# Optimization experiments

Measured on AMD Instinct MI355X. Metric: run time of the kernel, lower is better.

Reference implementation:

```python
import jax, jax.numpy as jnp
import numpy as np

B, S, D, H = 4, 2048, 1024, 16
HD = D // H  # head dim = 64
NEG = jnp.finfo(jnp.float32).min


def setup_inputs() -> dict:
    key = jax.random.key(0)
    ks = jax.random.split(key, 6)
    states = jax.random.normal(ks[0], (B, S, D), dtype=jnp.float32)
    # causal float mask, broadcastable over batch and heads
    mask = jnp.tril(jnp.ones((S, S), dtype=jnp.float32))[None, None, :, :]
    scale = 1.0 / np.sqrt(D)
    Wq = jax.random.normal(ks[1], (D, D), dtype=jnp.float32) * scale
    Wk = jax.random.normal(ks[2], (D, D), dtype=jnp.float32) * scale
    Wv = jax.random.normal(ks[3], (D, D), dtype=jnp.float32) * scale
    Wo = jax.random.normal(ks[4], (D, D), dtype=jnp.float32) * scale
    return {"states": states, "mask": mask, "Wq": Wq, "Wk": Wk, "Wv": Wv, "Wo": Wo}


def _split_heads(x):
    # [B,S,D] -> [B,H,S,HD]
    return x.reshape(B, S, H, HD).transpose(0, 2, 1, 3)


def reference(states, mask, Wq, Wk, Wv, Wo):
    q = _split_heads(states @ Wq)
    k = _split_heads(states @ Wk)
    v = _split_heads(states @ Wv)
    # scores [B,H,S,S], scaled by rsqrt(head_dim) as in the original
    alpha = jnp.einsum("bhqd,bhkd->bhqk", q, k) * (1.0 / jnp.sqrt(jnp.float32(HD)))
    alpha = alpha * mask + (1.0 - mask) * NEG
    alpha = jax.nn.softmax(alpha, axis=-1)
    ctx = jnp.einsum("bhqk,bhkd->bhqd", alpha, v)
    ctx = ctx.transpose(0, 2, 1, 3).reshape(B, S, D)  # concat heads
    return ctx @ Wo
```

## Files before the change

kernel.cpp:

```cpp
#include <hip/hip_runtime.h>
#include <hip/hip_bf16.h>

#define BB 4
#define SS 2048
#define DD 1024
#define HH 16
#define HDD 64
#define MM (BB*SS)

typedef __attribute__((ext_vector_type(8))) short short8;
typedef __attribute__((ext_vector_type(4))) float f32x4;
typedef __attribute__((ext_vector_type(4))) int int4v;
typedef __attribute__((ext_vector_type(4))) short bf16x4;

__device__ __forceinline__ ushort f2bf(float f) {
  union { float f; uint u; } v; v.f = f;
  uint u = v.u;
  uint r = (u + 0x7FFFu + ((u >> 16) & 1u)) >> 16;
  return (ushort)r;
}

__device__ __forceinline__ float exp2f_fast(float x) {
#if __has_builtin(__builtin_amdgcn_exp2f)
  return __builtin_amdgcn_exp2f(x);
#else
  float r; asm("v_exp_f32 %0, %1" : "=v"(r) : "v"(x)); return r;
#endif
}

__device__ __forceinline__ bf16x4 pack4bf(float a, float b, float c, float d) {
  union { __hip_bfloat162 h2[2]; bf16x4 s; } u;
  u.h2[0] = __float22bfloat162_rn(make_float2(a, b));
  u.h2[1] = __float22bfloat162_rn(make_float2(c, d));
  return u.s;
}

__device__ __forceinline__ f32x4 mfma16(bf16x4 a, bf16x4 b, f32x4 c) {
#if __has_builtin(__builtin_amdgcn_mfma_f32_16x16x16bf16_1k)
  return __builtin_amdgcn_mfma_f32_16x16x16bf16_1k(a, b, c, 0, 0, 0);
#else
  f32x4 d;
  asm volatile("s_nop 1\n\tv_mfma_f32_16x16x16_bf16 %0, %1, %2, %3\n\ts_nop 7\n\ts_nop 3"
               : "=v"(d) : "v"(a), "v"(b), "v"(c));
  return d;
#endif
}

__device__ __forceinline__ void gload16(void* lds, const void* g) {
  __builtin_amdgcn_global_load_lds((const __attribute__((address_space(1))) void*)g,
                                   (__attribute__((address_space(3))) void*)lds, 16, 0, 0);
}

__global__ __launch_bounds__(256) void k_prep(const float* __restrict__ states, ushort* __restrict__ Xbf,
                                              const float* __restrict__ W0, const float* __restrict__ W1,
                                              const float* __restrict__ W2, const float* __restrict__ W3,
                                              ushort* __restrict__ T0, ushort* __restrict__ T1,
                                              ushort* __restrict__ T2, ushort* __restrict__ T3) {
  int bid = blockIdx.x;
  int tid = threadIdx.x;
  if (bid >= 4096) {
    int i = (bid - 4096) * 256 + tid;
    float4 v = ((const float4*)states)[i];
    uint lo = (uint)f2bf(v.x) | ((uint)f2bf(v.y) << 16);
    uint hi = (uint)f2bf(v.z) | ((uint)f2bf(v.w) << 16);
    ((uint2*)Xbf)[i] = make_uint2(lo, hi);
    return;
  }
  __shared__ float t[32][33];
  int bz = bid >> 10;
  int by = (bid >> 5) & 31, bx = bid & 31;
  const float* W; ushort* T;
  switch (bz) {
    case 0: W = W0; T = T0; break;
    case 1: W = W1; T = T1; break;
    case 2: W = W2; T = T2; break;
    default: W = W3; T = T3; break;
  }
  float scale = (bz == 0) ? 0.18033688011112042f : 1.0f;
  int tx = tid & 31, ty = tid >> 5;
  int x = bx * 32 + tx;
  int y0 = by * 32;
#pragma unroll
  for (int j = 0; j < 32; j += 8) t[ty + j][tx] = W[(y0 + ty + j) * DD + x];
  __syncthreads();
#pragma unroll
  for (int j = 0; j < 32; j += 8)
    T[(bx * 32 + ty + j) * DD + y0 + tx] = f2bf(t[tx][ty + j] * scale);
}

__global__ __launch_bounds__(256, 2) void k_qkv(const ushort* __restrict__ X,
                                                const ushort* __restrict__ Wqt,
                                                const ushort* __restrict__ Wkt,
                                                const ushort* __restrict__ Wvt,
                                                ushort* __restrict__ Q,
                                                ushort* __restrict__ K,
                                                ushort* __restrict__ Vt) {
  __shared__ ushort Al[2 * 4096];
  __shared__ ushort Bl[3][2 * 4096];
  int tid = threadIdx.x, lane = tid & 63, w = tid >> 6;
  int wm = w >> 1, wn = w & 1, lrow = lane & 15, lgrp = lane >> 4;
  int srow = lane >> 2, scolb = (lane & 3) * 16;
  const char* A8 = (const char*)(X + (size_t)blockIdx.x * 128 * DD);
  const char* B8[3] = { (const char*)(Wqt + (size_t)blockIdx.y * 128 * DD),
                        (const char*)(Wkt + (size_t)blockIdx.y * 128 * DD),
                        (const char*)(Wvt + (size_t)blockIdx.y * 128 * DD) };

  f32x4 acc[3][4][4];
#pragma unroll
  for (int wi = 0; wi < 3; wi++)
#pragma unroll
    for (int i = 0; i < 4; i++)
#pragma unroll
      for (int j = 0; j < 4; j++)
#pragma unroll
        for (int r = 0; r < 4; r++) acc[wi][i][j][r] = 0.f;

#pragma unroll
  for (int ii = 0; ii < 2; ii++) {
    int i = w * 2 + ii;
    size_t ro = (size_t)(i * 16 + srow) * (DD * 2) + scolb;
    gload16(Al + i * 512, A8 + ro);
#pragma unroll
    for (int wi = 0; wi < 3; wi++)
      gload16(&Bl[wi][i * 512], B8[wi] + ro);
  }
  __syncthreads();

  for (int kk = 0; kk < DD; kk += 32) {
    int cur = (kk >> 5) & 1;
    if (kk + 32 < DD) {
#pragma unroll
      for (int ii = 0; ii < 2; ii++) {
        int i = w * 2 + ii;
        size_t ro = (size_t)(i * 16 + srow) * (DD * 2) + (kk + 32) * 2 + scolb;
        gload16(Al + (cur ^ 1) * 4096 + i * 512, A8 + ro);
#pragma unroll
        for (int wi = 0; wi < 3; wi++)
          gload16(&Bl[wi][(cur ^ 1) * 4096 + i * 512], B8[wi] + ro);
      }
    }
    short8 a[4];
#pragma unroll
    for (int i = 0; i < 4; i++)
      a[i] = *(const short8*)&Al[cur * 4096 + (wm * 64 + i * 16 + lrow) * 32 + lgrp * 8];
#pragma unroll
    for (int wi = 0; wi < 3; wi++) {
      short8 b[4];
#pragma unroll
      for (int j = 0; j < 4; j++)
        b[j] = *(const short8*)&Bl[wi][cur * 4096 + (wn * 64 + j * 16 + lrow) * 32 + lgrp * 8];
#pragma unroll
      for (int i = 0; i < 4; i++)
#pragma unroll
        for (int j = 0; j < 4; j++)
          acc[wi][i][j] = __builtin_amdgcn_mfma_f32_16x16x32_bf16(a[i], b[j], acc[wi][i][j], 0, 0, 0);
    }
    __syncthreads();
  }

  int m0 = blockIdx.x * 128 + wm * 64, n0 = blockIdx.y * 128 + wn * 64;
#pragma unroll
  for (int wi = 0; wi < 2; wi++) {
    ushort* Out = (wi == 0) ? Q : K;
#pragma unroll
    for (int i = 0; i < 4; i++)
#pragma unroll
      for (int j = 0; j < 4; j++)
#pragma unroll
        for (int r = 0; r < 4; r++) {
          int row = m0 + i * 16 + lgrp * 4 + r;
          int col = n0 + j * 16 + lrow;
          int b = row >> 11, s = row & 2047, h = col >> 6, hd = col & 63;
          Out[(((size_t)(b * HH + h) * SS) + s) * HDD + hd] = f2bf(acc[wi][i][j][r]);
        }
  }
#pragma unroll
  for (int i = 0; i < 4; i++)
#pragma unroll
    for (int j = 0; j < 4; j++) {
      int row0 = m0 + i * 16 + lgrp * 4;
      int col = n0 + j * 16 + lrow;
      int b = row0 >> 11, s0 = row0 & 2047, h = col >> 6, hd = col & 63;
      bf16x4 s = pack4bf(acc[2][i][j][0], acc[2][i][j][1], acc[2][i][j][2], acc[2][i][j][3]);
      *(bf16x4*)(Vt + (((size_t)(b * HH + h) * HDD) + hd) * SS + s0) = s;
    }
}

#define QB2 64
#define KVB 64
#define NQT2 (SS / QB2)

__global__ __launch_bounds__(128) void k_attn(const ushort* __restrict__ Q,
                                              const ushort* __restrict__ K,
                                              const ushort* __restrict__ Vt,
                                              ushort* __restrict__ Ctx) {
  __shared__ ushort Kl[2][4096];
  __shared__ ushort Vl[2][4096];
  int bid = blockIdx.x;
  int xcd = bid & 7, slot = bid >> 3;
  int j = slot & 15;
  int bh = (slot >> 4) * 8 + xcd;
  int b = bh >> 4, h = bh & 15;
  int tid = threadIdx.x, lane = tid & 63, w = tid >> 6;
  int lrow = lane & 15, lgrp = lane >> 4;

  int srow = lane >> 3;
  int scolb = ((lane & 7) * 16) ^ (srow << 4);
  const char* K8 = (const char*)(K + (size_t)bh * SS * HDD);
  const char* V8 = (const char*)(Vt + (size_t)bh * HDD * SS);

  int kswz = (lrow & 7) << 3;
  int colE[2];
  colE[0] = (lgrp * 8) ^ kswz;
  colE[1] = (lgrp * 8 + 32) ^ kswz;

  const ushort* kc0 = &Kl[0][lrow * 64 + colE[0]];
  const ushort* kc1 = &Kl[0][lrow * 64 + colE[1]];
  const ushort* vbp[4];
#pragma unroll
  for (int t = 0; t < 4; t++) vbp[t] = &Vl[0][lrow * 64 + (((16 * t + lgrp * 4) ^ kswz))];

#pragma unroll
  for (int ph = 0; ph < 2; ph++) {
    int qx = ph == 0 ? (NQT2 - 1 - j) : j;
    int qb = qx * QB2;
    int qw0 = qb + w * 32;
    int ntk = qx + 1;

    const char* kgp[4];
    const char* vgp[4];
#pragma unroll
    for (int ii = 0; ii < 4; ii++) {
      kgp[ii] = K8 + (size_t)(w * 32 + ii * 8 + srow) * 128 + scolb;
      vgp[ii] = V8 + (size_t)(w * 32 + ii * 8 + srow) * (SS * 2) + scolb;
    }

    short8 qf[2][2];
#pragma unroll
    for (int qt = 0; qt < 2; qt++)
#pragma unroll
      for (int c = 0; c < 2; c++)
        qf[qt][c] = *(const short8*)(Q + ((size_t)bh * SS + qb + w * 32 + qt * 16 + lrow) * HDD + lgrp * 8 + 32 * c);

    f32x4 o[2][4];
#pragma unroll
    for (int qt = 0; qt < 2; qt++)
#pragma unroll
      for (int nt = 0; nt < 4; nt++)
#pragma unroll
        for (int r = 0; r < 4; r++) o[qt][nt][r] = 0.f;
    float l_run[2] = {0.f, 0.f};

#pragma unroll
    for (int ii = 0; ii < 4; ii++) {
      gload16(&Kl[0][(w * 4 + ii) * 512], kgp[ii]);
      gload16(&Vl[0][(w * 4 + ii) * 512], vgp[ii]);
      kgp[ii] += KVB * 128;
      vgp[ii] += KVB * 2;
    }
    __syncthreads();

    for (int kt = 0; kt < ntk; kt++) {
      int cur = kt & 1;
      if (kt + 1 < ntk) {
#pragma unroll
        for (int ii = 0; ii < 4; ii++) {
          gload16(&Kl[cur ^ 1][(w * 4 + ii) * 512], kgp[ii]);
          gload16(&Vl[cur ^ 1][(w * 4 + ii) * 512], vgp[ii]);
          kgp[ii] += KVB * 128;
          vgp[ii] += KVB * 2;
        }
      }
      int kb = kt * KVB;
      const ushort* kcc0 = kc0 + (cur << 12);
      const ushort* kcc1 = kc1 + (cur << 12);
      short8 kf[4][2];
#pragma unroll
      for (int t = 0; t < 4; t++) {
        kf[t][0] = *(const short8*)(kcc0 + t * 1024);
        kf[t][1] = *(const short8*)(kcc1 + t * 1024);
      }

      bf16x4 pk[2][4];
#pragma unroll
      for (int qt = 0; qt < 2; qt++) {
        f32x4 st[4];
#pragma unroll
        for (int t = 0; t < 4; t++) {
          f32x4 z;
#pragma unroll
          for (int r = 0; r < 4; r++) z[r] = 0.f;
          z = __builtin_amdgcn_mfma_f32_16x16x32_bf16(kf[t][0], qf[qt][0], z, 0, 0, 0);
          z = __builtin_amdgcn_mfma_f32_16x16x32_bf16(kf[t][1], qf[qt][1], z, 0, 0, 0);
          st[t] = z;
        }
        if (kb + 63 > qw0) {
          int lim = qw0 + qt * 16 + lrow - kb - lgrp * 4;
#pragma unroll
          for (int t = 0; t < 4; t++)
#pragma unroll
            for (int r = 0; r < 4; r++)
              if (16 * t + r > lim) st[t][r] = -1e30f;
        }
        float rs = 0.f;
#pragma unroll
        for (int t = 0; t < 4; t++) {
          float e0 = exp2f_fast(st[t][0] - 8.f);
          float e1 = exp2f_fast(st[t][1] - 8.f);
          float e2 = exp2f_fast(st[t][2] - 8.f);
          float e3 = exp2f_fast(st[t][3] - 8.f);
          rs += (e0 + e1) + (e2 + e3);
          pk[qt][t] = pack4bf(e0, e1, e2, e3);
        }
        l_run[qt] += rs;
      }

#pragma unroll
      for (int t = 0; t < 4; t++) {
        const ushort* vbt = vbp[t] + (cur << 12);
#pragma unroll
        for (int nt = 0; nt < 4; nt++) {
          bf16x4 va = *(const bf16x4*)(vbt + nt * 1024);
          o[0][nt] = mfma16(va, pk[0][t], o[0][nt]);
          o[1][nt] = mfma16(va, pk[1][t], o[1][nt]);
        }
      }
      __syncthreads();
    }

#pragma unroll
    for (int qt = 0; qt < 2; qt++) {
      float lt = l_run[qt];
      lt += __shfl_xor(lt, 16);
      lt += __shfl_xor(lt, 32);
      float inv = 1.f / lt;
      int q = qb + w * 32 + qt * 16 + lrow;
      ushort* base = Ctx + ((size_t)b * SS + q) * DD + h * HDD;
#pragma unroll
      for (int nt = 0; nt < 4; nt++) {
        bf16x4 s = pack4bf(o[qt][nt][0] * inv, o[qt][nt][1] * inv,
                           o[qt][nt][2] * inv, o[qt][nt][3] * inv);
        *(bf16x4*)(base + nt * 16 + lgrp * 4) = s;
      }
    }
  }
}

__global__ __launch_bounds__(256) void k_oproj(const ushort* __restrict__ Ctx,
                                               const ushort* __restrict__ Wot,
                                               float* __restrict__ Outp) {
  __shared__ ushort Al[2][8192];
  __shared__ ushort Bl[2][8192];
  int tid = threadIdx.x, lane = tid & 63, w = tid >> 6;
  int wm = w >> 1, wn = w & 1, lrow = lane & 15, lgrp = lane >> 4;
  int srow = lane >> 3;
  int scolb = ((lane & 7) * 16) ^ (srow << 4);
  const char* A8 = (const char*)(Ctx + (size_t)blockIdx.x * 128 * DD);
  const char* B8 = (const char*)(Wot + (size_t)blockIdx.y * 128 * DD);

  f32x4 acc[4][4];
#pragma unroll
  for (int i = 0; i < 4; i++)
#pragma unroll
    for (int j = 0; j < 4; j++)
#pragma unroll
      for (int r = 0; r < 4; r++) acc[i][j][r] = 0.f;

  int aswz = (lrow & 7) << 3;
  int colA[2], colB[2];
#pragma unroll
  for (int k2 = 0; k2 < 2; k2++) {
    colA[k2] = (k2 * 32 + lgrp * 8) ^ aswz;
    colB[k2] = (k2 * 32 + lgrp * 8) ^ aswz;
  }

#pragma unroll
  for (int ii = 0; ii < 4; ii++) {
    int i = w * 4 + ii;
    size_t ro = (size_t)(i * 8 + srow) * (DD * 2) + scolb;
    gload16(&Al[0][i * 512], A8 + ro);
    gload16(&Bl[0][i * 512], B8 + ro);
  }
  __syncthreads();

  for (int kk = 0; kk < DD; kk += 64) {
    int cur = (kk >> 6) & 1;
    if (kk + 64 < DD) {
#pragma unroll
      for (int ii = 0; ii < 4; ii++) {
        int i = w * 4 + ii;
        size_t ro = (size_t)(i * 8 + srow) * (DD * 2) + (kk + 64) * 2 + scolb;
        gload16(&Al[cur ^ 1][i * 512], A8 + ro);
        gload16(&Bl[cur ^ 1][i * 512], B8 + ro);
      }
    }
    short8 a[4][2], bfr[4][2];
#pragma unroll
    for (int i = 0; i < 4; i++)
#pragma unroll
      for (int k2 = 0; k2 < 2; k2++)
        a[i][k2] = *(const short8*)&Al[cur][(wm * 64 + i * 16 + lrow) * 64 + colA[k2]];
#pragma unroll
    for (int jj = 0; jj < 4; jj++)
#pragma unroll
      for (int k2 = 0; k2 < 2; k2++)
        bfr[jj][k2] = *(const short8*)&Bl[cur][(wn * 64 + jj * 16 + lrow) * 64 + colB[k2]];
#pragma unroll
    for (int i = 0; i < 4; i++)
#pragma unroll
      for (int jj = 0; jj < 4; jj++) {
        acc[i][jj] = __builtin_amdgcn_mfma_f32_16x16x32_bf16(a[i][0], bfr[jj][0], acc[i][jj], 0, 0, 0);
        acc[i][jj] = __builtin_amdgcn_mfma_f32_16x16x32_bf16(a[i][1], bfr[jj][1], acc[i][jj], 0, 0, 0);
      }
    __syncthreads();
  }

  int m0 = blockIdx.x * 128 + wm * 64, n0 = blockIdx.y * 128 + wn * 64;
#pragma unroll
  for (int i = 0; i < 4; i++)
#pragma unroll
    for (int j = 0; j < 4; j++)
#pragma unroll
      for (int r = 0; r < 4; r++) {
        int row = m0 + i * 16 + lgrp * 4 + r;
        int col = n0 + j * 16 + lrow;
        Outp[(size_t)row * DD + col] = acc[i][j][r];
      }
}

extern "C" void kernel_launch(void* const* d_in, const int* in_sizes, int n_in,
                              void* d_out, int out_size, void* d_ws, size_t ws_size,
                              hipStream_t stream) {
  const float* states = (const float*)d_in[0];
  const float* Wq = (const float*)d_in[2];
  const float* Wk = (const float*)d_in[3];
  const float* Wv = (const float*)d_in[4];
  const float* Wo = (const float*)d_in[5];
  float* outp = (float*)d_out;

  char* ws = (char*)d_ws;
  const size_t XBF = 0;
  const size_t WQT = 16777216;
  const size_t WKT = WQT + 2097152;
  const size_t WVT = WKT + 2097152;
  const size_t WOT = WVT + 2097152;
  const size_t QO  = WOT + 2097152;
  const size_t KO  = QO + 16777216;
  const size_t VT  = KO + 16777216;
  const size_t CTX = VT + 16777216;

  ushort* Xbf = (ushort*)(ws + XBF);
  ushort* Wqt = (ushort*)(ws + WQT);
  ushort* Wkt = (ushort*)(ws + WKT);
  ushort* Wvt = (ushort*)(ws + WVT);
  ushort* Wot = (ushort*)(ws + WOT);
  ushort* Qb  = (ushort*)(ws + QO);
  ushort* Kb  = (ushort*)(ws + KO);
  ushort* Vtb = (ushort*)(ws + VT);
  ushort* Ctb = (ushort*)(ws + CTX);

  k_prep<<<dim3(4096 + MM * DD / 4 / 256), 256, 0, stream>>>(
      states, Xbf, Wq, Wk, Wv, Wo, Wqt, Wkt, Wvt, Wot);
  k_qkv<<<dim3(MM / 128, DD / 128), 256, 0, stream>>>(Xbf, Wqt, Wkt, Wvt, Qb, Kb, Vtb);
  k_attn<<<dim3(NQT2 * BB * HH / 2), 128, 0, stream>>>(Qb, Kb, Vtb, Ctb);
  k_oproj<<<dim3(MM / 128, DD / 128), 256, 0, stream>>>(Ctb, Wot, outp);
}
```

Measured before the change: 158.1 us.

## Deepen attention K/V pipeline to four 32-key stages with explicit vmcnt waits

The attention kernel now processes 32-key tiles through a four-slot shared-memory ring, prefetching three tiles ahead. It replaces the trailing __syncthreads with explicit s_waitcnt vmcnt plus a single s_barrier per iteration. The V tile layout and swizzle are reworked for 32-column tiles. This aims to hide global-load latency better in the latency-bound attention loop, at the cost of twice as many loop iterations and barriers and hand-tuned wait counts that must match the load count. The oproj changes are cosmetic: colB is merged into colA and the grid expression is rewritten to the same value.

```diff
diff --git a/kernel.cpp b/kernel.cpp
--- a/kernel.cpp
+++ b/kernel.cpp
@@ -187,15 +187,15 @@
 }
 
 #define QB2 64
-#define KVB 64
+#define KVB3 32
 #define NQT2 (SS / QB2)
 
 __global__ __launch_bounds__(128) void k_attn(const ushort* __restrict__ Q,
                                               const ushort* __restrict__ K,
                                               const ushort* __restrict__ Vt,
                                               ushort* __restrict__ Ctx) {
-  __shared__ ushort Kl[2][4096];
-  __shared__ ushort Vl[2][4096];
+  __shared__ ushort Kl[4][2048];
+  __shared__ ushort Vl[4][2048];
   int bid = blockIdx.x;
   int xcd = bid & 7, slot = bid >> 3;
   int j = slot & 15;
@@ -206,6 +206,8 @@
 
   int srow = lane >> 3;
   int scolb = ((lane & 7) * 16) ^ (srow << 4);
+  int vrow = lane >> 2;
+  int vcolb = ((lane & 3) * 16) ^ ((vrow & 3) << 4);
   const char* K8 = (const char*)(K + (size_t)bh * SS * HDD);
   const char* V8 = (const char*)(Vt + (size_t)bh * HDD * SS);
 
@@ -216,23 +218,22 @@
 
   const ushort* kc0 = &Kl[0][lrow * 64 + colE[0]];
   const ushort* kc1 = &Kl[0][lrow * 64 + colE[1]];
-  const ushort* vbp[4];
-#pragma unroll
-  for (int t = 0; t < 4; t++) vbp[t] = &Vl[0][lrow * 64 + (((16 * t + lgrp * 4) ^ kswz))];
+  const ushort* vb0 = &Vl[0][lrow * 32 + (( 0 + 4 * lgrp) ^ ((lrow & 3) << 3))];
+  const ushort* vb1 = &Vl[0][lrow * 32 + ((16 + 4 * lgrp) ^ ((lrow & 3) << 3))];
 
 #pragma unroll
   for (int ph = 0; ph < 2; ph++) {
     int qx = ph == 0 ? (NQT2 - 1 - j) : j;
     int qb = qx * QB2;
     int qw0 = qb + w * 32;
-    int ntk = qx + 1;
-
-    const char* kgp[4];
-    const char* vgp[4];
-#pragma unroll
-    for (int ii = 0; ii < 4; ii++) {
-      kgp[ii] = K8 + (size_t)(w * 32 + ii * 8 + srow) * 128 + scolb;
-      vgp[ii] = V8 + (size_t)(w * 32 + ii * 8 + srow) * (SS * 2) + scolb;
+    int ntk = 2 * (qx + 1);
+
+    const char* kgp[2];
+    const char* vgp[2];
+#pragma unroll
+    for (int ii = 0; ii < 2; ii++) {
+      kgp[ii] = K8 + (size_t)((w * 2 + ii) * 8 + srow) * 128 + scolb;
+      vgp[ii] = V8 + (size_t)((w * 2 + ii) * 16 + vrow) * (SS * 2) + vcolb;
     }
 
     short8 qf[2][2];
@@ -240,7 +241,7 @@
     for (int qt = 0; qt < 2; qt++)
 #pragma unroll
       for (int c = 0; c < 2; c++)
-        qf[qt][c] = *(const short8*)(Q + ((size_t)bh * SS + qb + w * 32 + qt * 16 + lrow) * HDD + lgrp * 8 + 32 * c);
+        qf[qt][c] = *(const short8*)(Q + ((size_t)bh * SS + qw0 + qt * 16 + lrow) * HDD + lgrp * 8 + 32 * c);
 
     f32x4 o[2][4];
 #pragma unroll
@@ -251,42 +252,52 @@
         for (int r = 0; r < 4; r++) o[qt][nt][r] = 0.f;
     float l_run[2] = {0.f, 0.f};
 
-#pragma unroll
-    for (int ii = 0; ii < 4; ii++) {
-      gload16(&Kl[0][(w * 4 + ii) * 512], kgp[ii]);
-      gload16(&Vl[0][(w * 4 + ii) * 512], vgp[ii]);
-      kgp[ii] += KVB * 128;
-      vgp[ii] += KVB * 2;
-    }
-    __syncthreads();
+    int npro = ntk < 3 ? ntk : 3;
+    for (int s = 0; s < npro; s++) {
+#pragma unroll
+      for (int ii = 0; ii < 2; ii++) {
+        gload16(&Kl[s][(w * 2 + ii) * 512], kgp[ii]);
+        gload16(&Vl[s][(w * 2 + ii) * 512], vgp[ii]);
+        kgp[ii] += KVB3 * 128;
+        vgp[ii] += KVB3 * 2;
+      }
+    }
 
     for (int kt = 0; kt < ntk; kt++) {
-      int cur = kt & 1;
-      if (kt + 1 < ntk) {
-#pragma unroll
-        for (int ii = 0; ii < 4; ii++) {
-          gload16(&Kl[cur ^ 1][(w * 4 + ii) * 512], kgp[ii]);
-          gload16(&Vl[cur ^ 1][(w * 4 + ii) * 512], vgp[ii]);
-          kgp[ii] += KVB * 128;
-          vgp[ii] += KVB * 2;
+      int rem = ntk - kt;
+      if (rem >= 3)      { asm volatile("s_waitcnt vmcnt(8)" ::: "memory"); }
+      else if (rem == 2) { asm volatile("s_waitcnt vmcnt(4)" ::: "memory"); }
+      else               { asm volatile("s_waitcnt vmcnt(0)" ::: "memory"); }
+      __builtin_amdgcn_sched_barrier(0);
+      __builtin_amdgcn_s_barrier();
+      __builtin_amdgcn_sched_barrier(0);
+      if (kt + 3 < ntk) {
+        int nb = (kt + 3) & 3;
+#pragma unroll
+        for (int ii = 0; ii < 2; ii++) {
+          gload16(&Kl[nb][(w * 2 + ii) * 512], kgp[ii]);
+          gload16(&Vl[nb][(w * 2 + ii) * 512], vgp[ii]);
+          kgp[ii] += KVB3 * 128;
+          vgp[ii] += KVB3 * 2;
         }
       }
-      int kb = kt * KVB;
-      const ushort* kcc0 = kc0 + (cur << 12);
-      const ushort* kcc1 = kc1 + (cur << 12);
-      short8 kf[4][2];
-#pragma unroll
-      for (int t = 0; t < 4; t++) {
+      int buf = kt & 3;
+      int kb = kt * KVB3;
+      const ushort* kcc0 = kc0 + (buf << 11);
+      const ushort* kcc1 = kc1 + (buf << 11);
+      short8 kf[2][2];
+#pragma unroll
+      for (int t = 0; t < 2; t++) {
         kf[t][0] = *(const short8*)(kcc0 + t * 1024);
         kf[t][1] = *(const short8*)(kcc1 + t * 1024);
       }
 
-      bf16x4 pk[2][4];
+      bf16x4 pk[2][2];
 #pragma unroll
       for (int qt = 0; qt < 2; qt++) {
-        f32x4 st[4];
-#pragma unroll
-        for (int t = 0; t < 4; t++) {
+        f32x4 st[2];
+#pragma unroll
+        for (int t = 0; t < 2; t++) {
           f32x4 z;
 #pragma unroll
           for (int r = 0; r < 4; r++) z[r] = 0.f;
@@ -294,17 +305,17 @@
           z = __builtin_amdgcn_mfma_f32_16x16x32_bf16(kf[t][1], qf[qt][1], z, 0, 0, 0);
           st[t] = z;
         }
-        if (kb + 63 > qw0) {
+        if (kb + 31 > qw0) {
           int lim = qw0 + qt * 16 + lrow - kb - lgrp * 4;
 #pragma unroll
-          for (int t = 0; t < 4; t++)
+          for (int t = 0; t < 2; t++)
 #pragma unroll
             for (int r = 0; r < 4; r++)
               if (16 * t + r > lim) st[t][r] = -1e30f;
         }
         float rs = 0.f;
 #pragma unroll
-        for (int t = 0; t < 4; t++) {
+        for (int t = 0; t < 2; t++) {
           float e0 = exp2f_fast(st[t][0] - 8.f);
           float e1 = exp2f_fast(st[t][1] - 8.f);
           float e2 = exp2f_fast(st[t][2] - 8.f);
@@ -315,17 +326,17 @@
         l_run[qt] += rs;
       }
 
-#pragma unroll
-      for (int t = 0; t < 4; t++) {
-        const ushort* vbt = vbp[t] + (cur << 12);
-#pragma unroll
-        for (int nt = 0; nt < 4; nt++) {
-          bf16x4 va = *(const bf16x4*)(vbt + nt * 1024);
-          o[0][nt] = mfma16(va, pk[0][t], o[0][nt]);
-          o[1][nt] = mfma16(va, pk[1][t], o[1][nt]);
-        }
-      }
-      __syncthreads();
+      const ushort* vbt0 = vb0 + (buf << 11);
+      const ushort* vbt1 = vb1 + (buf << 11);
+#pragma unroll
+      for (int nt = 0; nt < 4; nt++) {
+        bf16x4 va0 = *(const bf16x4*)(vbt0 + nt * 512);
+        bf16x4 va1 = *(const bf16x4*)(vbt1 + nt * 512);
+        o[0][nt] = mfma16(va0, pk[0][0], o[0][nt]);
+        o[1][nt] = mfma16(va0, pk[1][0], o[1][nt]);
+        o[0][nt] = mfma16(va1, pk[0][1], o[0][nt]);
+        o[1][nt] = mfma16(va1, pk[1][1], o[1][nt]);
+      }
     }
 
 #pragma unroll
@@ -334,7 +345,7 @@
       lt += __shfl_xor(lt, 16);
       lt += __shfl_xor(lt, 32);
       float inv = 1.f / lt;
-      int q = qb + w * 32 + qt * 16 + lrow;
+      int q = qw0 + qt * 16 + lrow;
       ushort* base = Ctx + ((size_t)b * SS + q) * DD + h * HDD;
 #pragma unroll
       for (int nt = 0; nt < 4; nt++) {
@@ -343,8 +354,10 @@
         *(bf16x4*)(base + nt * 16 + lgrp * 4) = s;
       }
     }
-  }
-}
+    __builtin_amdgcn_s_barrier();
+  }
+}
+
 
 __global__ __launch_bounds__(256) void k_oproj(const ushort* __restrict__ Ctx,
                                                const ushort* __restrict__ Wot,
@@ -367,12 +380,9 @@
       for (int r = 0; r < 4; r++) acc[i][j][r] = 0.f;
 
   int aswz = (lrow & 7) << 3;
-  int colA[2], colB[2];
-#pragma unroll
-  for (int k2 = 0; k2 < 2; k2++) {
-    colA[k2] = (k2 * 32 + lgrp * 8) ^ aswz;
-    colB[k2] = (k2 * 32 + lgrp * 8) ^ aswz;
-  }
+  int colA[2];
+  colA[0] = (lgrp * 8) ^ aswz;
+  colA[1] = (32 + lgrp * 8) ^ aswz;
 
 #pragma unroll
   for (int ii = 0; ii < 4; ii++) {
@@ -404,7 +414,7 @@
     for (int jj = 0; jj < 4; jj++)
 #pragma unroll
       for (int k2 = 0; k2 < 2; k2++)
-        bfr[jj][k2] = *(const short8*)&Bl[cur][(wn * 64 + jj * 16 + lrow) * 64 + colB[k2]];
+        bfr[jj][k2] = *(const short8*)&Bl[cur][(wn * 64 + jj * 16 + lrow) * 64 + colA[k2]];
 #pragma unroll
     for (int i = 0; i < 4; i++)
 #pragma unroll
@@ -463,5 +473,5 @@
       states, Xbf, Wq, Wk, Wv, Wo, Wqt, Wkt, Wvt, Wot);
   k_qkv<<<dim3(MM / 128, DD / 128), 256, 0, stream>>>(Xbf, Wqt, Wkt, Wvt, Qb, Kb, Vtb);
   k_attn<<<dim3(NQT2 * BB * HH / 2), 128, 0, stream>>>(Qb, Kb, Vtb, Ctb);
-  k_oproj<<<dim3(MM / 128, DD / 128), 256, 0, stream>>>(Ctb, Wot, outp);
-}
+  k_oproj<<<dim3(MM / 128, DD / 256 * 2), 256, 0, stream>>>(Ctb, Wot, outp);
+}
```

Result: slower. 175.2 us (+10.9%).
